# Optimization experiments

Hardware: AMD Instinct MI355X
Metric: run time of the kernel (lower is better)

The kernel has to match this reference:

```python
import jax, jax.numpy as jnp
import numpy as np

B, S, F = 64, 512, 64      # batch, encoder seq len, input features
H = 512                    # encoder hidden == decoder hidden (required by Attention)
U = 128                    # attention units
T_OUT, OUT_F = 96, 1       # output horizon, output features


def _p(key, shape, scale=0.05):
    return scale * jax.random.normal(key, shape, dtype=jnp.float32)


def setup_inputs() -> dict:
    key = jax.random.key(0)
    ks = jax.random.split(key, 18)
    d = {
        "x": jax.random.normal(ks[0], (B, S, F), dtype=jnp.float32),
        # encoder LSTM (torch gate order i,f,g,o)
        "enc_Wih": _p(ks[1], (4 * H, F)),
        "enc_Whh": _p(ks[2], (4 * H, H)),
        "enc_bih": _p(ks[3], (4 * H,)),
        "enc_bhh": _p(ks[4], (4 * H,)),
        # attention
        "att_W1": _p(ks[5], (U, H)),
        "att_b1": _p(ks[6], (U,)),
        "att_W2": _p(ks[7], (U, H)),
        "att_b2": _p(ks[8], (U,)),
        "att_V": _p(ks[9], (1, U)),
        "att_bV": _p(ks[10], (1,)),
        # decoder LSTM: input = cat(context[H], y_t[OUT_F])
        "dec_Wih": _p(ks[11], (4 * H, H + OUT_F)),
        "dec_Whh": _p(ks[12], (4 * H, H)),
        "dec_bih": _p(ks[13], (4 * H,)),
        "dec_bhh": _p(ks[14], (4 * H,)),
        # output projection
        "out_W": _p(ks[15], (OUT_F, H)),
        "out_b": _p(ks[16], (OUT_F,)),
    }
    return d


def _lstm_gates(pre):
    i, f, g, o = jnp.split(pre, 4, axis=-1)
    return jax.nn.sigmoid(i), jax.nn.sigmoid(f), jnp.tanh(g), jax.nn.sigmoid(o)


def _forward(x, enc_Wih, enc_Whh, enc_bih, enc_bhh,
             att_W1, att_b1, att_W2, att_b2, att_V, att_bV,
             dec_Wih, dec_Whh, dec_bih, dec_bhh, out_W, out_b):
    b = x.shape[0]
    # ---- encoder LSTM over S steps ----
    x_pre = jnp.einsum('bsf,gf->bsg', x, enc_Wih) + enc_bih + enc_bhh  # precompute input GEMM

    def enc_step(carry, xp_t):
        h, c = carry
        i, f, g, o = _lstm_gates(xp_t + h @ enc_Whh.T)
        c = f * c + i * g
        h = o * jnp.tanh(c)
        return (h, c), h

    h0 = jnp.zeros((b, H), x.dtype)
    (enc_hn, _), enc_out = jax.lax.scan(enc_step, (h0, h0), jnp.swapaxes(x_pre, 0, 1))
    enc_out = jnp.swapaxes(enc_out, 0, 1)  # [B,S,H]

    # W2(enc_out) is step-invariant -> hoist out of the decode loop
    w2_enc = jnp.einsum('bsh,uh->bsu', enc_out, att_W2) + att_b2  # [B,S,U]

    # y is None in inference path -> teacher-forcing inputs are zeros
    y_t = jnp.zeros((b, OUT_F), x.dtype)
    dec_bias = dec_bih + dec_bhh  # h0=c0=0 each decoder call (torch code passes no state)

    def dec_step(h_att, _):
        # Bahdanau attention
        w1_h = h_att @ att_W1.T + att_b1                       # [B,U]
        score = jnp.tanh(w1_h[:, None, :] + w2_enc) @ att_V.T + att_bV  # [B,S,1]
        attn = jax.nn.softmax(score, axis=1)
        ctx = jnp.sum(attn * enc_out, axis=1)                  # [B,H]
        # single decoder LSTM cell step from zero state
        x_t = jnp.concatenate([ctx, y_t], axis=-1)             # [B,H+OUT_F]
        i, f, g, o = _lstm_gates(x_t @ dec_Wih.T + dec_bias)   # f*c0 = 0, Whh@h0 = 0
        c = i * g
        h = o * jnp.tanh(c)
        out_t = h @ out_W.T + out_b                            # [B,OUT_F]
        return h, out_t

    _, outs = jax.lax.scan(dec_step, enc_hn, None, length=T_OUT)
    return jnp.swapaxes(outs, 0, 1)  # [B,T_OUT,OUT_F]


def reference(x, enc_Wih, enc_Whh, enc_bih, enc_bhh,
              att_W1, att_b1, att_W2, att_b2, att_V, att_bV,
              dec_Wih, dec_Whh, dec_bih, dec_bhh, out_W, out_b):
    return _forward(x, enc_Wih, enc_Whh, enc_bih, enc_bhh,
                    att_W1, att_b1, att_W2, att_b2, att_V, att_bV,
                    dec_Wih, dec_Whh, dec_bih, dec_bhh, out_W, out_b)
```

## Files before the change

### kernel.cpp

```cpp
#include <hip/hip_runtime.h>

#define Bn 64
#define Sn 512
#define Fn 64
#define Hn 512
#define Un 128
#define Tn 96

typedef __attribute__((ext_vector_type(8))) short bf16x8;
typedef __attribute__((ext_vector_type(4))) float f32x4;
typedef unsigned int u32;

#define MFMA16(a, b, c) __builtin_amdgcn_mfma_f32_16x16x32_bf16(a, b, c, 0, 0, 0)

__device__ __forceinline__ float sigm(float x) { return 1.0f / (1.0f + __expf(-x)); }
__device__ __forceinline__ float tanh_f(float x) {
    x = fminf(fmaxf(x, -15.0f), 15.0f);
    float e = __expf(2.0f * x);
    return (e - 1.0f) / (e + 1.0f);
}
__device__ __forceinline__ short bf16rtn(float f) {
    unsigned u = __float_as_uint(f);
    unsigned r = (u + 0x7FFFu + ((u >> 16) & 1u)) >> 16;
    return (short)r;
}
__device__ __forceinline__ float bf16tof(short s) {
    return __uint_as_float(((unsigned)(unsigned short)s) << 16);
}

__global__ __launch_bounds__(256) void k_split_x(const float* __restrict__ x,
                                                 short* __restrict__ xhi, short* __restrict__ xlo) {
    int t = blockIdx.x * 256 + threadIdx.x;
    int f = t & 63, s = (t >> 6) & 511, b = t >> 15;
    float v = x[t];
    short hi = bf16rtn(v);
    short lo = bf16rtn(v - bf16tof(hi));
    int o = (s * Bn + b) * Fn + f;
    xhi[o] = hi; xlo[o] = lo;
}
__global__ __launch_bounds__(256) void k_split_whh(const float* __restrict__ w,
                                                   short* __restrict__ whi, short* __restrict__ wlo) {
    int t = blockIdx.x * 256 + threadIdx.x;
    int k = t & 511, r = t >> 9;
    int g = r >> 9, j = r & 511;
    float v = w[t];
    short hi = bf16rtn(v);
    short lo = bf16rtn(v - bf16tof(hi));
    int o = (j * 4 + g) * 512 + k;
    whi[o] = hi; wlo[o] = lo;
}
__global__ __launch_bounds__(256) void k_split_wih(const float* __restrict__ w,
                                                   short* __restrict__ whi, short* __restrict__ wlo) {
    int t = blockIdx.x * 256 + threadIdx.x;
    int k = t & 63, r = t >> 6;
    int g = r >> 9, j = r & 511;
    float v = w[t];
    short hi = bf16rtn(v);
    short lo = bf16rtn(v - bf16tof(hi));
    int o = (j * 4 + g) * 64 + k;
    whi[o] = hi; wlo[o] = lo;
}
__global__ __launch_bounds__(256) void k_bias_perm(const float* __restrict__ bih,
                                                   const float* __restrict__ bhh,
                                                   float* __restrict__ bperm) {
    int t = blockIdx.x * 256 + threadIdx.x;
    int g = t >> 9, j = t & 511;
    bperm[j * 4 + g] = bih[t] + bhh[t];
}
__global__ __launch_bounds__(256) void k_w1t(const float* __restrict__ W1, float* __restrict__ W1T) {
    int t = blockIdx.x * 256 + threadIdx.x;
    int u = t >> 9, k = t & 511;
    W1T[k * Un + u] = W1[t];
}
__global__ __launch_bounds__(256) void k_w2t_bf16(const float* __restrict__ W2, short* __restrict__ W2Tb) {
    int t = blockIdx.x * 256 + threadIdx.x;
    int u = t >> 9, j = t & 511;
    W2Tb[j * Un + u] = bf16rtn(W2[t]);
}
__global__ __launch_bounds__(256) void k_transpose_dec(const float* __restrict__ dW, float* __restrict__ WiT,
                                                       float* __restrict__ WgT, float* __restrict__ WoT) {
    int t = blockIdx.x * 256 + threadIdx.x;
    int j = t & 511, j2 = t >> 9;
    WiT[t] = dW[(j)        * 513 + j2];
    WgT[t] = dW[(1024 + j) * 513 + j2];
    WoT[t] = dW[(1536 + j) * 513 + j2];
}
__global__ __launch_bounds__(256) void k_zero_state(float* __restrict__ hz, float* __restrict__ se) {
    int t = blockIdx.x * 256 + threadIdx.x;
    if (t < 98304) hz[t] = 0.0f;
    else se[t - 98304] = 0.0f;
}

__global__ __launch_bounds__(512)
void enc_step3(const short* __restrict__ xhi, const short* __restrict__ xlo,
               const short* __restrict__ whhHi, const short* __restrict__ whhLo,
               const short* __restrict__ wihHi, const short* __restrict__ wihLo,
               const float* __restrict__ bperm,
               const short* __restrict__ hHiP, const short* __restrict__ hLoP,
               short* __restrict__ hHiN, short* __restrict__ hLoN,
               float* __restrict__ cstG, short* __restrict__ encJ, int t)
{
    const int mt = blockIdx.x >> 1, nt = blockIdx.x & 1;
    const int tid = threadIdx.x;
    const int wv = tid >> 6, l = tid & 63;
    const int nw = wv & 1, kw = wv >> 1;
    const int lr = l & 15, lk = l >> 4;
    const int row  = mt * 16 + lr;
    const int bcol = nt * 32 + nw * 16 + lr;

    f32x4 acc = {0.f, 0.f, 0.f, 0.f};
    if (kw < 2) {
        int k0 = kw * 32 + lk * 8;
        bf16x8 XBh = *(const bf16x8*)(xhi + ((size_t)t * 64 + bcol) * 64 + k0);
        bf16x8 XBl = *(const bf16x8*)(xlo + ((size_t)t * 64 + bcol) * 64 + k0);
        bf16x8 Ah  = *(const bf16x8*)(wihHi + (size_t)row * 64 + k0);
        bf16x8 Al  = *(const bf16x8*)(wihLo + (size_t)row * 64 + k0);
        acc = MFMA16(Ah, XBh, acc);
        acc = MFMA16(Ah, XBl, acc);
        acc = MFMA16(Al, XBh, acc);
    }
    #pragma unroll
    for (int c = 0; c < 4; c++) {
        int k0 = kw * 128 + c * 32 + lk * 8;
        bf16x8 Ah = *(const bf16x8*)(whhHi + (size_t)row * 512 + k0);
        bf16x8 Al = *(const bf16x8*)(whhLo + (size_t)row * 512 + k0);
        bf16x8 Bh = *(const bf16x8*)(hHiP + (size_t)bcol * 512 + k0);
        bf16x8 Bl = *(const bf16x8*)(hLoP + (size_t)bcol * 512 + k0);
        acc = MFMA16(Ah, Bh, acc);
        acc = MFMA16(Ah, Bl, acc);
        acc = MFMA16(Al, Bh, acc);
    }
    __shared__ float red[3][2][64][4];
    if (kw) *(f32x4*)(&red[kw - 1][nw][l][0]) = acc;
    __syncthreads();
    if (kw == 0) {
        f32x4 r0 = *(const f32x4*)(&red[0][nw][l][0]);
        f32x4 r1 = *(const f32x4*)(&red[1][nw][l][0]);
        f32x4 r2 = *(const f32x4*)(&red[2][nw][l][0]);
        const int jloc = mt * 4 + lk;
        const f32x4 bias = *(const f32x4*)(bperm + mt * 16 + lk * 4);
        float pi = acc[0] + r0[0] + r1[0] + r2[0] + bias[0];
        float pf = acc[1] + r0[1] + r1[1] + r2[1] + bias[1];
        float pg = acc[2] + r0[2] + r1[2] + r2[2] + bias[2];
        float po = acc[3] + r0[3] + r1[3] + r2[3] + bias[3];
        float ig = sigm(pi), fg = sigm(pf), gg = tanh_f(pg), og = sigm(po);
        float cn = fg * cstG[jloc * Bn + bcol] + ig * gg;
        float hv = og * tanh_f(cn);
        cstG[jloc * Bn + bcol] = cn;
        short hi16 = bf16rtn(hv);
        short lo16 = bf16rtn(hv - bf16tof(hi16));
        hHiN[bcol * 512 + jloc] = hi16;
        hLoN[bcol * 512 + jloc] = lo16;
        encJ[(size_t)jloc * (Sn * Bn) + t * Bn + bcol] = hi16;
    }
}

__global__ __launch_bounds__(256)
void w2enc_k(const short* __restrict__ encJ, const short* __restrict__ W2Tb,
             const float* __restrict__ b2, short* __restrict__ w2eb)
{
    __shared__ float tile[64 * 64];
    const int s = blockIdx.x;
    const int tid = threadIdx.x;
    const int u = tid & 127, bq = tid >> 7;
    float acc[32];
    #pragma unroll
    for (int i = 0; i < 32; i++) acc[i] = 0.f;
    for (int jc = 0; jc < 8; jc++) {
        __syncthreads();
        #pragma unroll
        for (int r = 0; r < 16; r++) {
            int e = r * 256 + tid;
            int jl = e >> 6, b = e & 63;
            tile[e] = bf16tof(encJ[(jc * 64 + jl) * (Sn * Bn) + s * Bn + b]);
        }
        __syncthreads();
        for (int jl = 0; jl < 64; jl++) {
            float wv = bf16tof(W2Tb[(jc * 64 + jl) * Un + u]);
            const float4* trow = (const float4*)&tile[jl * 64 + bq * 32];
            #pragma unroll
            for (int i = 0; i < 8; i++) {
                float4 t4 = trow[i];
                acc[i*4+0] += t4.x * wv; acc[i*4+1] += t4.y * wv;
                acc[i*4+2] += t4.z * wv; acc[i*4+3] += t4.w * wv;
            }
        }
    }
    float bb = b2[u];
    #pragma unroll
    for (int i = 0; i < 32; i++)
        w2eb[(((size_t)(bq * 32 + i)) * Sn + s) * Un + u] = bf16rtn(acc[i] + bb);
}

__global__ __launch_bounds__(256)
void dec_attn_k(const float* __restrict__ hdec, const short* __restrict__ encJ,
                const float* __restrict__ W1T, const float* __restrict__ b1,
                const float* __restrict__ Vv, const float* __restrict__ bV,
                const short* __restrict__ w2eb, const float* __restrict__ oW,
                const float* __restrict__ ob, float* __restrict__ eT,
                float* __restrict__ sumE, float* __restrict__ out, int t)
{
    __shared__ float hs[512];
    __shared__ float w1h[Un];
    __shared__ float Vs[Un];
    __shared__ float red2[256];
    const int tid = threadIdx.x;
    const int b = blockIdx.x >> 2, sc = blockIdx.x & 3;

    if (t == 0) {
        hs[tid]       = bf16tof(encJ[tid * (Sn * Bn) + (Sn - 1) * Bn + b]);
        hs[tid + 256] = bf16tof(encJ[(tid + 256) * (Sn * Bn) + (Sn - 1) * Bn + b]);
    } else {
        hs[tid]       = hdec[tid * Bn + b];
        hs[tid + 256] = hdec[(tid + 256) * Bn + b];
    }
    if (tid < 128) Vs[tid] = Vv[tid];
    __syncthreads();

    if (sc == 0 && t > 0) {
        red2[tid] = oW[tid] * hs[tid] + oW[tid + 256] * hs[tid + 256];
        __syncthreads();
        for (int w = 128; w > 0; w >>= 1) { if (tid < w) red2[tid] += red2[tid + w]; __syncthreads(); }
        if (tid == 0) out[b * Tn + (t - 1)] = red2[0] + ob[0];
        __syncthreads();
    }

    {
        const int u = tid & 127, kh = tid >> 7;
        float a = 0.f;
        #pragma unroll 8
        for (int k = 0; k < 256; k++) {
            int kk = kh * 256 + k;
            a += W1T[kk * Un + u] * hs[kk];
        }
        red2[tid] = a;
    }
    __syncthreads();
    if (tid < 128) w1h[tid] = red2[tid] + red2[tid + 128] + b1[tid];
    __syncthreads();

    const int sl = sc * 128 + (tid >> 1), uh = tid & 1;
    const short* r  = w2eb + ((size_t)b * Sn + sl) * Un + uh * 64;
    const float* wp = w1h + uh * 64;
    const float* vp = Vs + uh * 64;
    float s0 = 0.f;
    #pragma unroll
    for (int q = 0; q < 8; q++) {
        bf16x8 v8 = *(const bf16x8*)(r + q * 8);
        #pragma unroll
        for (int e2 = 0; e2 < 8; e2++)
            s0 += vp[q * 8 + e2] * tanh_f(wp[q * 8 + e2] + bf16tof(v8[e2]));
    }
    s0 += __shfl_xor(s0, 1);
    float e = 0.f;
    if (uh == 0) {
        e = __expf(s0 + bV[0]);
        eT[sl * Bn + b] = e;
    }
    __syncthreads();
    red2[tid] = e;
    __syncthreads();
    for (int w = 128; w > 0; w >>= 1) { if (tid < w) red2[tid] += red2[tid + w]; __syncthreads(); }
    if (tid == 0) atomicAdd(&sumE[t * Bn + b], red2[0]);
}

__global__ __launch_bounds__(256)
void dec_ctx_k(const float* __restrict__ eT, const short* __restrict__ encJ,
               float* __restrict__ ctx)
{
    const int tid = threadIdx.x;
    const int j = blockIdx.x;
    const int b = tid & 63, sq = tid >> 6;
    const short* ep = encJ + j * (Sn * Bn) + b;
    float a = 0.f;
    #pragma unroll 8
    for (int s = sq * 128; s < sq * 128 + 128; s++)
        a += eT[s * Bn + b] * bf16tof(ep[s * Bn]);
    __shared__ float red[256];
    red[tid] = a;
    __syncthreads();
    if (sq == 0) ctx[j * Bn + b] = red[b] + red[64 + b] + red[128 + b] + red[192 + b];
}

__global__ __launch_bounds__(256)
void dec_gate_k(const float* __restrict__ ctx, const float* __restrict__ sumE,
                const float* __restrict__ WiT, const float* __restrict__ WgT,
                const float* __restrict__ WoT, const float* __restrict__ dbih,
                const float* __restrict__ dbhh, float* __restrict__ hdec, int t)
{
    const int tid = threadIdx.x;
    const int b = tid & 63, kq = tid >> 6;
    const int j = blockIdx.x;
    float ai = 0.f, ag = 0.f, ao = 0.f;
    #pragma unroll 4
    for (int k = kq * 128; k < kq * 128 + 128; k++) {
        float cv = ctx[k * Bn + b];
        ai += WiT[k * Hn + j] * cv;
        ag += WgT[k * Hn + j] * cv;
        ao += WoT[k * Hn + j] * cv;
    }
    __shared__ float red[3][4][64];
    red[0][kq][b] = ai; red[1][kq][b] = ag; red[2][kq][b] = ao;
    __syncthreads();
    if (kq == 0) {
        float inv = 1.0f / sumE[t * Bn + b];
        float pi = (red[0][0][b] + red[0][1][b] + red[0][2][b] + red[0][3][b]) * inv + dbih[j] + dbhh[j];
        float pg = (red[1][0][b] + red[1][1][b] + red[1][2][b] + red[1][3][b]) * inv + dbih[2*Hn + j] + dbhh[2*Hn + j];
        float po = (red[2][0][b] + red[2][1][b] + red[2][2][b] + red[2][3][b]) * inv + dbih[3*Hn + j] + dbhh[3*Hn + j];
        float cc = sigm(pi) * tanh_f(pg);
        float hh = sigm(po) * tanh_f(cc);
        hdec[j * Bn + b] = hh;
    }
}

__global__ __launch_bounds__(64)
void dec_out_k(const float* __restrict__ hdec, const float* __restrict__ oW,
               const float* __restrict__ ob, float* __restrict__ out, int t)
{
    const int b = blockIdx.x;
    const int tid = threadIdx.x;
    float a = 0.f;
    #pragma unroll
    for (int q = 0; q < 8; q++) {
        int j = tid + q * 64;
        a += oW[j] * hdec[j * Bn + b];
    }
    for (int off = 32; off; off >>= 1) a += __shfl_down(a, off, 64);
    if (tid == 0) out[b * Tn + t] = a + ob[0];
}

extern "C" void kernel_launch(void* const* d_in, const int* in_sizes, int n_in,
                              void* d_out, int out_size, void* d_ws, size_t ws_size,
                              hipStream_t stream) {
    const float* x    = (const float*)d_in[0];
    const float* eWih = (const float*)d_in[1];
    const float* eWhh = (const float*)d_in[2];
    const float* ebih = (const float*)d_in[3];
    const float* ebhh = (const float*)d_in[4];
    const float* aW1  = (const float*)d_in[5];
    const float* ab1  = (const float*)d_in[6];
    const float* aW2  = (const float*)d_in[7];
    const float* ab2  = (const float*)d_in[8];
    const float* aV   = (const float*)d_in[9];
    const float* abV  = (const float*)d_in[10];
    const float* dWih = (const float*)d_in[11];
    const float* dbih = (const float*)d_in[13];
    const float* dbhh = (const float*)d_in[14];
    const float* oW   = (const float*)d_in[15];
    const float* ob   = (const float*)d_in[16];
    float* out = (float*)d_out;

    char* wsb = (char*)d_ws;
    short* xhi    = (short*)(wsb + 0);
    short* xlo    = (short*)(wsb + 4194304);
    short* whhHi  = (short*)(wsb + 8388608);
    short* whhLo  = (short*)(wsb + 10485760);
    short* wihHi  = (short*)(wsb + 12582912);
    short* wihLo  = (short*)(wsb + 12845056);
    float* bperm  = (float*)(wsb + 13107200);
    short* W2Tb   = (short*)(wsb + 13115392);
    float* W1T    = (float*)(wsb + 13246464);
    float* WiT    = (float*)(wsb + 13508608);
    float* WgT    = (float*)(wsb + 14557184);
    float* WoT    = (float*)(wsb + 15605760);
    short* hHi    = (short*)(wsb + 16654336);
    short* hLo    = (short*)(wsb + 16785408);
    float* cstG   = (float*)(wsb + 16916480);
    short* encJ   = (short*)(wsb + 17047552);
    short* w2eb   = (short*)(wsb + 50601984);
    float* eT     = (float*)(wsb + 58990592);
    float* sumE   = (float*)(wsb + 59121664);
    float* ctx    = (float*)(wsb + 59146240);
    float* hdec   = (float*)(wsb + 59277312);

    k_split_x      <<<8192, 256, 0, stream>>>(x, xhi, xlo);
    k_split_whh    <<<4096, 256, 0, stream>>>(eWhh, whhHi, whhLo);
    k_split_wih    <<<512,  256, 0, stream>>>(eWih, wihHi, wihLo);
    k_bias_perm    <<<8,    256, 0, stream>>>(ebih, ebhh, bperm);
    k_w1t          <<<256,  256, 0, stream>>>(aW1, W1T);
    k_w2t_bf16     <<<256,  256, 0, stream>>>(aW2, W2Tb);
    k_transpose_dec<<<1024, 256, 0, stream>>>(dWih, WiT, WgT, WoT);
    k_zero_state   <<<408,  256, 0, stream>>>((float*)hHi, sumE);

    for (int t = 0; t < Sn; t++) {
        const int pr = t & 1, pw = 1 - pr;
        enc_step3<<<256, 512, 0, stream>>>(xhi, xlo, whhHi, whhLo, wihHi, wihLo,
                                           bperm,
                                           hHi + pr * 32768, hLo + pr * 32768,
                                           hHi + pw * 32768, hLo + pw * 32768,
                                           cstG, encJ, t);
    }

    w2enc_k<<<512, 256, 0, stream>>>(encJ, W2Tb, ab2, w2eb);

    for (int t = 0; t < Tn; t++) {
        dec_attn_k<<<256, 256, 0, stream>>>(hdec, encJ, W1T, ab1, aV, abV, w2eb,
                                            oW, ob, eT, sumE, out, t);
        dec_ctx_k <<<512, 256, 0, stream>>>(eT, encJ, ctx);
        dec_gate_k<<<512, 256, 0, stream>>>(ctx, sumE, WiT, WgT, WoT, dbih, dbhh, hdec, t);
    }
    dec_out_k<<<64, 64, 0, stream>>>(hdec, oW, ob, out, Tn - 1);
}
```

Measured before the change: 7.503 ms.

## Fuse setup kernels, store W1 as bf16, read decoder weights untransposed

Merges the eight setup kernels into one launch and drops the decoder weight transpose. The decoder gate kernel now reads dec_Wih directly with 8 output columns per 512-thread block. W1 is stored as bf16 to halve the attention weight reads. The aim is fewer launches and less setup traffic, but the per-lane weight loads in the gate kernel are scalar broadcasts with a 513 stride, and only 64 blocks run per step, which may hurt the decoder loop.

```diff
diff --git a/kernel.cpp b/kernel.cpp
--- a/kernel.cpp
+++ b/kernel.cpp
@@ -28,67 +28,61 @@
     return __uint_as_float(((unsigned)(unsigned short)s) << 16);
 }
 
-__global__ __launch_bounds__(256) void k_split_x(const float* __restrict__ x,
-                                                 short* __restrict__ xhi, short* __restrict__ xlo) {
+__global__ __launch_bounds__(256)
+void k_setup_all(const float* __restrict__ x, const float* __restrict__ whh,
+                 const float* __restrict__ wih, const float* __restrict__ bih,
+                 const float* __restrict__ bhh, const float* __restrict__ W1,
+                 const float* __restrict__ W2,
+                 short* __restrict__ xhi, short* __restrict__ xlo,
+                 short* __restrict__ whhHi, short* __restrict__ whhLo,
+                 short* __restrict__ wihHi, short* __restrict__ wihLo,
+                 float* __restrict__ bperm, short* __restrict__ W1Tb,
+                 short* __restrict__ W2Tb, float* __restrict__ hz,
+                 float* __restrict__ se)
+{
     int t = blockIdx.x * 256 + threadIdx.x;
-    int f = t & 63, s = (t >> 6) & 511, b = t >> 15;
-    float v = x[t];
-    short hi = bf16rtn(v);
-    short lo = bf16rtn(v - bf16tof(hi));
-    int o = (s * Bn + b) * Fn + f;
-    xhi[o] = hi; xlo[o] = lo;
-}
-__global__ __launch_bounds__(256) void k_split_whh(const float* __restrict__ w,
-                                                   short* __restrict__ whi, short* __restrict__ wlo) {
-    int t = blockIdx.x * 256 + threadIdx.x;
-    int k = t & 511, r = t >> 9;
-    int g = r >> 9, j = r & 511;
-    float v = w[t];
-    short hi = bf16rtn(v);
-    short lo = bf16rtn(v - bf16tof(hi));
-    int o = (j * 4 + g) * 512 + k;
-    whi[o] = hi; wlo[o] = lo;
-}
-__global__ __launch_bounds__(256) void k_split_wih(const float* __restrict__ w,
-                                                   short* __restrict__ whi, short* __restrict__ wlo) {
-    int t = blockIdx.x * 256 + threadIdx.x;
-    int k = t & 63, r = t >> 6;
-    int g = r >> 9, j = r & 511;
-    float v = w[t];
-    short hi = bf16rtn(v);
-    short lo = bf16rtn(v - bf16tof(hi));
-    int o = (j * 4 + g) * 64 + k;
-    whi[o] = hi; wlo[o] = lo;
-}
-__global__ __launch_bounds__(256) void k_bias_perm(const float* __restrict__ bih,
-                                                   const float* __restrict__ bhh,
-                                                   float* __restrict__ bperm) {
-    int t = blockIdx.x * 256 + threadIdx.x;
-    int g = t >> 9, j = t & 511;
-    bperm[j * 4 + g] = bih[t] + bhh[t];
-}
-__global__ __launch_bounds__(256) void k_w1t(const float* __restrict__ W1, float* __restrict__ W1T) {
-    int t = blockIdx.x * 256 + threadIdx.x;
-    int u = t >> 9, k = t & 511;
-    W1T[k * Un + u] = W1[t];
-}
-__global__ __launch_bounds__(256) void k_w2t_bf16(const float* __restrict__ W2, short* __restrict__ W2Tb) {
-    int t = blockIdx.x * 256 + threadIdx.x;
-    int u = t >> 9, j = t & 511;
-    W2Tb[j * Un + u] = bf16rtn(W2[t]);
-}
-__global__ __launch_bounds__(256) void k_transpose_dec(const float* __restrict__ dW, float* __restrict__ WiT,
-                                                       float* __restrict__ WgT, float* __restrict__ WoT) {
-    int t = blockIdx.x * 256 + threadIdx.x;
-    int j = t & 511, j2 = t >> 9;
-    WiT[t] = dW[(j)        * 513 + j2];
-    WgT[t] = dW[(1024 + j) * 513 + j2];
-    WoT[t] = dW[(1536 + j) * 513 + j2];
-}
-__global__ __launch_bounds__(256) void k_zero_state(float* __restrict__ hz, float* __restrict__ se) {
-    int t = blockIdx.x * 256 + threadIdx.x;
-    if (t < 98304) hz[t] = 0.0f;
-    else se[t - 98304] = 0.0f;
+    if (t < 2097152) {
+        int f = t & 63, s = (t >> 6) & 511, b = t >> 15;
+        float v = x[t];
+        short hi = bf16rtn(v);
+        short lo = bf16rtn(v - bf16tof(hi));
+        int o = (s * Bn + b) * Fn + f;
+        xhi[o] = hi; xlo[o] = lo;
+    } else if (t < 3145728) {
+        t -= 2097152;
+        int k = t & 511, r = t >> 9;
+        int g = r >> 9, j = r & 511;
+        float v = whh[t];
+        short hi = bf16rtn(v);
+        short lo = bf16rtn(v - bf16tof(hi));
+        int o = (j * 4 + g) * 512 + k;
+        whhHi[o] = hi; whhLo[o] = lo;
+    } else if (t < 3276800) {
+        t -= 3145728;
+        int k = t & 63, r = t >> 6;
+        int g = r >> 9, j = r & 511;
+        float v = wih[t];
+        short hi = bf16rtn(v);
+        short lo = bf16rtn(v - bf16tof(hi));
+        int o = (j * 4 + g) * 64 + k;
+        wihHi[o] = hi; wihLo[o] = lo;
+    } else if (t < 3278848) {
+        t -= 3276800;
+        int g = t >> 9, j = t & 511;
+        bperm[j * 4 + g] = bih[t] + bhh[t];
+    } else if (t < 3344384) {
+        t -= 3278848;
+        int u = t >> 9, k = t & 511;
+        W1Tb[k * Un + u] = bf16rtn(W1[t]);
+    } else if (t < 3409920) {
+        t -= 3344384;
+        int u = t >> 9, j = t & 511;
+        W2Tb[j * Un + u] = bf16rtn(W2[t]);
+    } else if (t < 3514368) {
+        t -= 3409920;
+        if (t < 98304) hz[t] = 0.0f;
+        else se[t - 98304] = 0.0f;
+    }
 }
 
 __global__ __launch_bounds__(512)
@@ -194,7 +188,7 @@
 
 __global__ __launch_bounds__(256)
 void dec_attn_k(const float* __restrict__ hdec, const short* __restrict__ encJ,
-                const float* __restrict__ W1T, const float* __restrict__ b1,
+                const short* __restrict__ W1Tb, const float* __restrict__ b1,
                 const float* __restrict__ Vv, const float* __restrict__ bV,
                 const short* __restrict__ w2eb, const float* __restrict__ oW,
                 const float* __restrict__ ob, float* __restrict__ eT,
@@ -231,7 +225,7 @@
         #pragma unroll 8
         for (int k = 0; k < 256; k++) {
             int kk = kh * 256 + k;
-            a += W1T[kk * Un + u] * hs[kk];
+            a += bf16tof(W1Tb[kk * Un + u]) * hs[kk];
         }
         red2[tid] = a;
     }
@@ -282,34 +276,53 @@
     if (sq == 0) ctx[j * Bn + b] = red[b] + red[64 + b] + red[128 + b] + red[192 + b];
 }
 
-__global__ __launch_bounds__(256)
-void dec_gate_k(const float* __restrict__ ctx, const float* __restrict__ sumE,
-                const float* __restrict__ WiT, const float* __restrict__ WgT,
-                const float* __restrict__ WoT, const float* __restrict__ dbih,
-                const float* __restrict__ dbhh, float* __restrict__ hdec, int t)
-{
-    const int tid = threadIdx.x;
-    const int b = tid & 63, kq = tid >> 6;
-    const int j = blockIdx.x;
-    float ai = 0.f, ag = 0.f, ao = 0.f;
-    #pragma unroll 4
-    for (int k = kq * 128; k < kq * 128 + 128; k++) {
+__global__ __launch_bounds__(512)
+void dec_gate2_k(const float* __restrict__ ctx, const float* __restrict__ sumE,
+                 const float* __restrict__ dW, const float* __restrict__ dbih,
+                 const float* __restrict__ dbhh, float* __restrict__ hdec, int t)
+{
+    const int tid = threadIdx.x;
+    const int b = tid & 63;
+    const int kq = __builtin_amdgcn_readfirstlane(tid >> 6);
+    const int j0 = blockIdx.x * 8;
+    float ai[8] = {}, ag[8] = {}, ao[8] = {};
+    for (int k = kq * 64; k < kq * 64 + 64; k++) {
         float cv = ctx[k * Bn + b];
-        ai += WiT[k * Hn + j] * cv;
-        ag += WgT[k * Hn + j] * cv;
-        ao += WoT[k * Hn + j] * cv;
-    }
-    __shared__ float red[3][4][64];
-    red[0][kq][b] = ai; red[1][kq][b] = ag; red[2][kq][b] = ao;
+        #pragma unroll
+        for (int jj = 0; jj < 8; jj++) {
+            int j = j0 + jj;
+            ai[jj] += dW[(size_t)(j)        * 513 + k] * cv;
+            ag[jj] += dW[(size_t)(1024 + j) * 513 + k] * cv;
+            ao[jj] += dW[(size_t)(1536 + j) * 513 + k] * cv;
+        }
+    }
+    __shared__ float red[8][24][64];
+    #pragma unroll
+    for (int jj = 0; jj < 8; jj++) {
+        red[kq][jj * 3 + 0][b] = ai[jj];
+        red[kq][jj * 3 + 1][b] = ag[jj];
+        red[kq][jj * 3 + 2][b] = ao[jj];
+    }
     __syncthreads();
     if (kq == 0) {
         float inv = 1.0f / sumE[t * Bn + b];
-        float pi = (red[0][0][b] + red[0][1][b] + red[0][2][b] + red[0][3][b]) * inv + dbih[j] + dbhh[j];
-        float pg = (red[1][0][b] + red[1][1][b] + red[1][2][b] + red[1][3][b]) * inv + dbih[2*Hn + j] + dbhh[2*Hn + j];
-        float po = (red[2][0][b] + red[2][1][b] + red[2][2][b] + red[2][3][b]) * inv + dbih[3*Hn + j] + dbhh[3*Hn + j];
-        float cc = sigm(pi) * tanh_f(pg);
-        float hh = sigm(po) * tanh_f(cc);
-        hdec[j * Bn + b] = hh;
+        #pragma unroll
+        for (int jj = 0; jj < 8; jj++) {
+            int j = j0 + jj;
+            float pi = 0.f, pg = 0.f, po = 0.f;
+            #pragma unroll
+            for (int q = 0; q < 8; q++) {
+                pi += red[q][jj * 3 + 0][b];
+                pg += red[q][jj * 3 + 1][b];
+                po += red[q][jj * 3 + 2][b];
+            }
+            pi = pi * inv + dbih[j]          + dbhh[j];
+            pg = pg * inv + dbih[2*Hn + j]   + dbhh[2*Hn + j];
+            po = po * inv + dbih[3*Hn + j]   + dbhh[3*Hn + j];
+            float cc = sigm(pi) * tanh_f(pg);
+            float hh = sigm(po) * tanh_f(cc);
+            hdec[j * Bn + b] = hh;
+        }
     }
 }
 
@@ -359,10 +372,7 @@
     short* wihLo  = (short*)(wsb + 12845056);
     float* bperm  = (float*)(wsb + 13107200);
     short* W2Tb   = (short*)(wsb + 13115392);
-    float* W1T    = (float*)(wsb + 13246464);
-    float* WiT    = (float*)(wsb + 13508608);
-    float* WgT    = (float*)(wsb + 14557184);
-    float* WoT    = (float*)(wsb + 15605760);
+    short* W1Tb   = (short*)(wsb + 13246464);
     short* hHi    = (short*)(wsb + 16654336);
     short* hLo    = (short*)(wsb + 16785408);
     float* cstG   = (float*)(wsb + 16916480);
@@ -373,14 +383,9 @@
     float* ctx    = (float*)(wsb + 59146240);
     float* hdec   = (float*)(wsb + 59277312);
 
-    k_split_x      <<<8192, 256, 0, stream>>>(x, xhi, xlo);
-    k_split_whh    <<<4096, 256, 0, stream>>>(eWhh, whhHi, whhLo);
-    k_split_wih    <<<512,  256, 0, stream>>>(eWih, wihHi, wihLo);
-    k_bias_perm    <<<8,    256, 0, stream>>>(ebih, ebhh, bperm);
-    k_w1t          <<<256,  256, 0, stream>>>(aW1, W1T);
-    k_w2t_bf16     <<<256,  256, 0, stream>>>(aW2, W2Tb);
-    k_transpose_dec<<<1024, 256, 0, stream>>>(dWih, WiT, WgT, WoT);
-    k_zero_state   <<<408,  256, 0, stream>>>((float*)hHi, sumE);
+    k_setup_all<<<13728, 256, 0, stream>>>(x, eWhh, eWih, ebih, ebhh, aW1, aW2,
+                                           xhi, xlo, whhHi, whhLo, wihHi, wihLo,
+                                           bperm, W1Tb, W2Tb, (float*)hHi, sumE);
 
     for (int t = 0; t < Sn; t++) {
         const int pr = t & 1, pw = 1 - pr;
@@ -394,10 +399,10 @@
     w2enc_k<<<512, 256, 0, stream>>>(encJ, W2Tb, ab2, w2eb);
 
     for (int t = 0; t < Tn; t++) {
-        dec_attn_k<<<256, 256, 0, stream>>>(hdec, encJ, W1T, ab1, aV, abV, w2eb,
+        dec_attn_k<<<256, 256, 0, stream>>>(hdec, encJ, W1Tb, ab1, aV, abV, w2eb,
                                             oW, ob, eT, sumE, out, t);
-        dec_ctx_k <<<512, 256, 0, stream>>>(eT, encJ, ctx);
-        dec_gate_k<<<512, 256, 0, stream>>>(ctx, sumE, WiT, WgT, WoT, dbih, dbhh, hdec, t);
+        dec_ctx_k  <<<512, 256, 0, stream>>>(eT, encJ, ctx);
+        dec_gate2_k<<<64,  512, 0, stream>>>(ctx, sumE, dWih, dbih, dbhh, hdec, t);
     }
     dec_out_k<<<64, 64, 0, stream>>>(hdec, oW, ob, out, Tn - 1);
 }
```

New measurement: 9.968 ms. 1.33x slower.
